# Kernel optimization log

Hardware: AMD Instinct MI355X
Metric: run time of the kernel (lower is better)

Reference implementation:

```python
import jax, jax.numpy as jnp
import numpy as np

EPS = 1e-5
NUM_HEAD = 8
HEAD_DIM = 64
SCALE = HEAD_DIM ** -0.5


def setup_inputs() -> dict:
    key = jax.random.key(0)
    ks = jax.random.split(key, 3)
    b, n, dim = 4, 2048, 512
    inner = NUM_HEAD * HEAD_DIM  # 512
    x = jax.random.normal(ks[0], (b, n, dim), dtype=jnp.float32)
    ln_w = jnp.ones((dim,), jnp.float32)
    ln_b = jnp.zeros((dim,), jnp.float32)
    qkv_w = jax.random.normal(ks[1], (3 * inner, dim), jnp.float32) * (dim ** -0.5)
    qkv_b = jnp.zeros((3 * inner,), jnp.float32)
    out_w = jax.random.normal(ks[2], (dim, inner), jnp.float32) * (inner ** -0.5)
    out_b = jnp.zeros((dim,), jnp.float32)
    return {"x": x, "ln_w": ln_w, "ln_b": ln_b, "qkv_w": qkv_w,
            "qkv_b": qkv_b, "out_w": out_w, "out_b": out_b}


def reference(x, ln_w, ln_b, qkv_w, qkv_b, out_w, out_b):
    b, n, dim = x.shape
    # Pre-norm LayerNorm
    mu = jnp.mean(x, axis=-1, keepdims=True)
    var = jnp.mean(jnp.square(x - mu), axis=-1, keepdims=True)
    xn = (x - mu) * jax.lax.rsqrt(var + EPS) * ln_w + ln_b
    # QKV projection (torch Linear: y = x @ W.T + b)
    qkv = xn @ qkv_w.T + qkv_b  # [b, n, 3*inner]
    q, k, v = jnp.split(qkv, 3, axis=-1)
    def heads(t):  # [b, n, inner] -> [b, h, n, d]
        return t.reshape(b, n, NUM_HEAD, HEAD_DIM).transpose(0, 2, 1, 3)
    q, k, v = heads(q), heads(k), heads(v)
    # Naive full attention (materializes [b, h, n, n])
    dots = jnp.einsum('bhqd,bhkd->bhqk', q, k) * SCALE
    attn = jax.nn.softmax(dots, axis=-1)
    o = jnp.einsum('bhqk,bhkd->bhqd', attn, v)
    o = o.transpose(0, 2, 1, 3).reshape(b, n, NUM_HEAD * HEAD_DIM)
    return o @ out_w.T + out_b
```

## Files before the change

### kernel.cpp

```cpp
#include <hip/hip_runtime.h>

typedef __attribute__((ext_vector_type(8))) short bf16x8;
typedef __attribute__((ext_vector_type(4))) float floatx4;
typedef __attribute__((ext_vector_type(16))) float floatx16;
typedef __attribute__((ext_vector_type(4))) unsigned int uintx4;

#define B_    4
#define N_    2048
#define DIM_  512
#define NH_   8
#define HD_   64
#define SCALE_ 0.125f
#define SL2E_ (0.125f * 1.44269504f)

__device__ __forceinline__ unsigned short f32_to_bf16(float f) {
    return (unsigned short)((__float_as_uint(f) + 0x8000u) >> 16);
}

__device__ __forceinline__ float bf16_to_f32(unsigned short u) {
    return __uint_as_float(((unsigned int)u) << 16);
}

__device__ __forceinline__ floatx4 mfma16(bf16x8 a, bf16x8 b, floatx4 c) {
    return __builtin_amdgcn_mfma_f32_16x16x32_bf16(a, b, c, 0, 0, 0);
}

__device__ __forceinline__ floatx16 mfma32(bf16x8 a, bf16x8 b, floatx16 c) {
    return __builtin_amdgcn_mfma_f32_32x32x16_bf16(a, b, c, 0, 0, 0);
}

__device__ __forceinline__ floatx4 fzero4() {
    floatx4 z = {0.f, 0.f, 0.f, 0.f};
    return z;
}

__device__ __forceinline__ floatx16 fzero16() {
    floatx16 z;
#pragma unroll
    for (int i = 0; i < 16; i++) z[i] = 0.f;
    return z;
}

__device__ __forceinline__ unsigned int cvt_pk_bf16(float lo, float hi) {
    unsigned int r;
    asm("v_cvt_pk_bf16_f32 %0, %1, %2" : "=v"(r) : "v"(lo), "v"(hi));
    return r;
}

__device__ __forceinline__ void async16(const unsigned short* g, unsigned short* l) {
    __builtin_amdgcn_global_load_lds((const __attribute__((address_space(1))) void*)g,
                                     (__attribute__((address_space(3))) void*)l,
                                     16, 0, 0);
}

__global__ __launch_bounds__(256) void ln_cvt_kernel(const float* __restrict__ x,
                                                     const float* __restrict__ w,
                                                     const float* __restrict__ b,
                                                     unsigned short* __restrict__ xn,
                                                     const float* __restrict__ srcA,
                                                     const float* __restrict__ srcB,
                                                     unsigned short* __restrict__ dstA,
                                                     unsigned short* __restrict__ dstB) {
    const int NWQ = 3 * DIM_ * DIM_;
    if (blockIdx.x < 2048) {
        int wv = threadIdx.x >> 6;
        int lane = threadIdx.x & 63;
        int row = blockIdx.x * 4 + wv;
        const float4* xr = (const float4*)(x + (size_t)row * DIM_);
        float4 v0 = xr[lane * 2];
        float4 v1 = xr[lane * 2 + 1];
        float s  = (v0.x + v0.y + v0.z + v0.w) + (v1.x + v1.y + v1.z + v1.w);
        float sq = v0.x*v0.x + v0.y*v0.y + v0.z*v0.z + v0.w*v0.w +
                   v1.x*v1.x + v1.y*v1.y + v1.z*v1.z + v1.w*v1.w;
#pragma unroll
        for (int off = 1; off < 64; off <<= 1) {
            s  += __shfl_xor(s, off, 64);
            sq += __shfl_xor(sq, off, 64);
        }
        float mu   = s * (1.f / DIM_);
        float var  = sq * (1.f / DIM_) - mu * mu;
        float rstd = rsqrtf(var + 1e-5f);
        float4 w0 = ((const float4*)w)[lane * 2];
        float4 w1 = ((const float4*)w)[lane * 2 + 1];
        float4 b0 = ((const float4*)b)[lane * 2];
        float4 b1 = ((const float4*)b)[lane * 2 + 1];
        float y[8];
        y[0] = (v0.x - mu) * rstd * w0.x + b0.x;
        y[1] = (v0.y - mu) * rstd * w0.y + b0.y;
        y[2] = (v0.z - mu) * rstd * w0.z + b0.z;
        y[3] = (v0.w - mu) * rstd * w0.w + b0.w;
        y[4] = (v1.x - mu) * rstd * w1.x + b1.x;
        y[5] = (v1.y - mu) * rstd * w1.y + b1.y;
        y[6] = (v1.z - mu) * rstd * w1.z + b1.z;
        y[7] = (v1.w - mu) * rstd * w1.w + b1.w;
        uint4 pk;
        pk.x = (unsigned int)f32_to_bf16(y[0]) | ((unsigned int)f32_to_bf16(y[1]) << 16);
        pk.y = (unsigned int)f32_to_bf16(y[2]) | ((unsigned int)f32_to_bf16(y[3]) << 16);
        pk.z = (unsigned int)f32_to_bf16(y[4]) | ((unsigned int)f32_to_bf16(y[5]) << 16);
        pk.w = (unsigned int)f32_to_bf16(y[6]) | ((unsigned int)f32_to_bf16(y[7]) << 16);
        ((uint4*)(xn + (size_t)row * DIM_))[lane] = pk;
    } else {
        int e0 = ((blockIdx.x - 2048) * 256 + threadIdx.x) * 8;
        const float* src;
        unsigned short* dst;
        if (e0 < NWQ) { src = srcA + e0; dst = dstA + e0; }
        else          { src = srcB + (e0 - NWQ); dst = dstB + (e0 - NWQ); }
        float4 u0 = ((const float4*)src)[0];
        float4 u1 = ((const float4*)src)[1];
        uint4 pk;
        pk.x = (unsigned int)f32_to_bf16(u0.x) | ((unsigned int)f32_to_bf16(u0.y) << 16);
        pk.y = (unsigned int)f32_to_bf16(u0.z) | ((unsigned int)f32_to_bf16(u0.w) << 16);
        pk.z = (unsigned int)f32_to_bf16(u1.x) | ((unsigned int)f32_to_bf16(u1.y) << 16);
        pk.w = (unsigned int)f32_to_bf16(u1.z) | ((unsigned int)f32_to_bf16(u1.w) << 16);
        *(uint4*)dst = pk;
    }
}

#define GEMM_CORE512(A_, B_ptr, am0, bn0)                                           \
    __shared__ unsigned short Alds[2][128][32];                                     \
    __shared__ unsigned short Blds[2][128][32];                                     \
    int tid = threadIdx.x, lane = tid & 63, wid = tid >> 6;                         \
    int l15 = lane & 15, quad = lane >> 4;                                          \
    int wmloc = (wid >> 1) * 32, wnloc = (wid & 1) * 64;                            \
    int sr = lane >> 2;                                                             \
    int sc = (lane & 3) * 8;                                                        \
    int srow0 = 16 * wid;                                                           \
    floatx4 acc[2][4];                                                              \
    _Pragma("unroll")                                                               \
    for (int i = 0; i < 2; i++)                                                     \
        _Pragma("unroll")                                                           \
        for (int j = 0; j < 4; j++) acc[i][j] = fzero4();                           \
    int buf = 0;                                                                    \
    async16(A_ + (size_t)(am0 + srow0 + sr) * DIM_ + sc, &Alds[0][srow0][0]);       \
    async16(B_ptr + (size_t)(bn0 + srow0 + sr) * DIM_ + sc, &Blds[0][srow0][0]);    \
    __syncthreads();                                                                \
    for (int t = 0; t < 16; t++) {                                                  \
        if (t < 15) {                                                               \
            int k0 = (t + 1) * 32;                                                  \
            async16(A_ + (size_t)(am0 + srow0 + sr) * DIM_ + k0 + sc,               \
                    &Alds[buf ^ 1][srow0][0]);                                      \
            async16(B_ptr + (size_t)(bn0 + srow0 + sr) * DIM_ + k0 + sc,            \
                    &Blds[buf ^ 1][srow0][0]);                                      \
        }                                                                           \
        bf16x8 av[2], bv[4];                                                        \
        _Pragma("unroll")                                                           \
        for (int i = 0; i < 2; i++)                                                 \
            av[i] = *(const bf16x8*)(&Alds[buf][wmloc + 16 * i + l15][quad * 8]);   \
        _Pragma("unroll")                                                           \
        for (int j = 0; j < 4; j++)                                                 \
            bv[j] = *(const bf16x8*)(&Blds[buf][wnloc + 16 * j + l15][quad * 8]);   \
        _Pragma("unroll")                                                           \
        for (int i = 0; i < 2; i++)                                                 \
            _Pragma("unroll")                                                       \
            for (int j = 0; j < 4; j++)                                             \
                acc[i][j] = mfma16(av[i], bv[j], acc[i][j]);                        \
        __syncthreads();                                                            \
        buf ^= 1;                                                                   \
    }

__global__ __launch_bounds__(512, 6) void qkv_gemm(const unsigned short* __restrict__ A,
                                                   const unsigned short* __restrict__ Bw,
                                                   const float* __restrict__ bias,
                                                   unsigned short* __restrict__ Qh,
                                                   unsigned short* __restrict__ Kh,
                                                   unsigned short* __restrict__ Vt) {
    int am0 = blockIdx.x * 128, bn0 = blockIdx.y * 128;
    GEMM_CORE512(A, Bw, am0, bn0)

    if (bn0 >= 1024) {
        unsigned short* sc_ = &Alds[0][0][0] + wid * (16 * 40);
        int m0 = am0 + wmloc;
        int bidx = m0 >> 11;
        int t0 = m0 & 2047;
#pragma unroll
        for (int j = 0; j < 4; j++) {
            float bias_n = bias[bn0 + wnloc + 16 * j + l15];
#pragma unroll
            for (int i = 0; i < 2; i++)
#pragma unroll
                for (int r = 0; r < 4; r++)
                    sc_[l15 * 40 + 16 * i + quad * 4 + r] =
                        f32_to_bf16(acc[i][j][r] + bias_n);
            int nr = lane >> 2;
            int rem = (bn0 - 1024) + wnloc + 16 * j + nr;
            int head = rem >> 6, d = rem & 63;
            bf16x8 vv = *(const bf16x8*)(sc_ + nr * 40 + (lane & 3) * 8);
            *(bf16x8*)(Vt + ((size_t)(bidx * NH_ + head) * HD_ + d) * N_ +
                       t0 + (lane & 3) * 8) = vv;
        }
    } else {
#pragma unroll
        for (int i = 0; i < 2; i++) {
#pragma unroll
            for (int j = 0; j < 4; j++) {
                int n = bn0 + wnloc + 16 * j + l15;
                float bias_n = bias[n];
                int which = n >> 9;
                int rem = n & 511;
                int head = rem >> 6;
                int d = rem & 63;
#pragma unroll
                for (int r = 0; r < 4; r++) {
                    int m = am0 + wmloc + 16 * i + quad * 4 + r;
                    int b = m >> 11;
                    int t = m & 2047;
                    float val = acc[i][j][r] + bias_n;
                    if (which == 0) {
                        Qh[((size_t)(b * NH_ + head) * N_ + t) * HD_ + d] =
                            f32_to_bf16(val * SL2E_);
                    } else {
                        Kh[((size_t)(b * NH_ + head) * N_ + t) * HD_ + d] =
                            f32_to_bf16(val);
                    }
                }
            }
        }
    }
}

__global__ __launch_bounds__(256, 4) void out_gemm_fused(const unsigned short* __restrict__ Opart,
                                                         const float* __restrict__ lpart,
                                                         const unsigned short* __restrict__ Bw,
                                                         const float* __restrict__ bias,
                                                         float* __restrict__ out) {
    __shared__ unsigned short Alds[2][64][36];
    __shared__ unsigned short Blds[2][128][32];
    int tid = threadIdx.x, lane = tid & 63, wid = tid >> 6;
    int l15 = lane & 15, quad = lane >> 4;
    int wmloc = (wid >> 1) * 32, wnloc = (wid & 1) * 64;
    int am0 = blockIdx.x * 64, bn0 = blockIdx.y * 128;

    int arow = tid >> 2;
    int ac8 = (tid & 3) * 8;
    int token = am0 + arow;
    int bb = token >> 11;
    const size_t LSTR = (size_t)B_ * NH_ * N_;
    const size_t OSTR = (size_t)B_ * N_ * DIM_;
    const unsigned short* arow0 = Opart + (size_t)token * DIM_;
    const unsigned short* arow1 = arow0 + OSTR;

    int sr = lane >> 2;
    int sc = (lane & 3) * 8;

    floatx4 acc[2][4];
#pragma unroll
    for (int i = 0; i < 2; i++)
#pragma unroll
        for (int j = 0; j < 4; j++) acc[i][j] = fzero4();

#define STAGE_A(BUF, T)                                                         \
    {                                                                           \
        int k0 = (T) * 32;                                                      \
        int head = k0 >> 6;                                                     \
        size_t li = (size_t)(bb * NH_ + head) * N_ + (token & 2047);            \
        float l1 = lpart[li];                                                   \
        float l2 = lpart[LSTR + li];                                            \
        float inv = 1.f / (l1 + l2);                                            \
        float w1 = l1 * inv, w2 = l2 * inv;                                     \
        bf16x8 o0 = *(const bf16x8*)(arow0 + k0 + ac8);                         \
        bf16x8 o1 = *(const bf16x8*)(arow1 + k0 + ac8);                         \
        bf16x8 pk;                                                              \
        _Pragma("unroll")                                                       \
        for (int e = 0; e < 8; e++)                                             \
            pk[e] = (short)f32_to_bf16(                                         \
                w1 * bf16_to_f32((unsigned short)o0[e]) +                       \
                w2 * bf16_to_f32((unsigned short)o1[e]));                       \
        *(bf16x8*)(&Alds[BUF][arow][ac8]) = pk;                                 \
    }

#define STAGE_B(BUF, T)                                                         \
    {                                                                           \
        int k0 = (T) * 32;                                                      \
        _Pragma("unroll")                                                       \
        for (int i = 0; i < 2; i++) {                                           \
            int r0 = 32 * wid + 16 * i;                                         \
            async16(Bw + (size_t)(bn0 + r0 + sr) * DIM_ + k0 + sc,              \
                    &Blds[BUF][r0][0]);                                         \
        }                                                                       \
    }

    STAGE_B(0, 0)
    STAGE_A(0, 0)
    __syncthreads();
    int buf = 0;
    for (int t = 0; t < 16; t++) {
        if (t < 15) {
            STAGE_B(buf ^ 1, t + 1)
            STAGE_A(buf ^ 1, t + 1)
        }
        bf16x8 av[2], bv[4];
#pragma unroll
        for (int i = 0; i < 2; i++)
            av[i] = *(const bf16x8*)(&Alds[buf][wmloc + 16 * i + l15][quad * 8]);
#pragma unroll
        for (int j = 0; j < 4; j++)
            bv[j] = *(const bf16x8*)(&Blds[buf][wnloc + 16 * j + l15][quad * 8]);
#pragma unroll
        for (int i = 0; i < 2; i++)
#pragma unroll
            for (int j = 0; j < 4; j++)
                acc[i][j] = mfma16(av[i], bv[j], acc[i][j]);
        __syncthreads();
        buf ^= 1;
    }
#undef STAGE_A
#undef STAGE_B

#pragma unroll
    for (int i = 0; i < 2; i++) {
#pragma unroll
        for (int j = 0; j < 4; j++) {
            int n = bn0 + wnloc + 16 * j + l15;
            float bias_n = bias[n];
#pragma unroll
            for (int r = 0; r < 4; r++) {
                int m = am0 + wmloc + 16 * i + quad * 4 + r;
                out[(size_t)m * DIM_ + n] = acc[i][j][r] + bias_n;
            }
        }
    }
}

__global__ __launch_bounds__(512, 4) void attn_kernel(const unsigned short* __restrict__ Qh,
                                                      const unsigned short* __restrict__ Kh,
                                                      const unsigned short* __restrict__ Vtg,
                                                      unsigned short* __restrict__ Opart,
                                                      float* __restrict__ lpart) {
    int bh = blockIdx.y;
    int b = bh >> 3, head = bh & 7;
    int qt = blockIdx.x;
    int split = blockIdx.z;
    int kv0 = split << 10;
    int tid = threadIdx.x, lane = tid & 63, w = tid >> 6;
    int l31 = lane & 31, hi = lane >> 5;
    int xr = l31 & 7;

    const unsigned short* Qp = Qh + (size_t)bh * N_ * HD_;
    const unsigned short* Kg = Kh + (size_t)bh * N_ * HD_;
    const unsigned short* Vg = Vtg + (size_t)bh * HD_ * N_;

    int q0 = qt * 256 + w * 32;

    bf16x8 aQ[4];
    {
        const unsigned short* qrow = Qp + (size_t)(q0 + l31) * HD_ + hi * 8;
#pragma unroll
        for (int t = 0; t < 4; t++)
            aQ[t] = *(const bf16x8*)(qrow + 16 * t);
    }

    __shared__ unsigned short KV[2][2][64][64];
    __shared__ float l_sm[8][32];

    int srow = lane >> 3;
    int scol = ((lane & 7) ^ srow) * 8;

    const char* ptc[4];
#pragma unroll
    for (int t = 0; t < 4; t++)
        ptc[t] = (const char*)&KV[0][0][l31][(((2 * t + hi) ^ xr) * 8)];

    const unsigned short* kSrc = Kg + (size_t)(kv0 + 8 * w + srow) * HD_ + scol;
    const unsigned short* vSrc = Vg + (size_t)(8 * w + srow) * N_ + kv0 + scol;

#define STAGE_KV(BUF, IT)                                                       \
    {                                                                           \
        async16(kSrc + (size_t)(IT) * 64 * HD_, &KV[BUF][0][8 * w][0]);         \
        async16(vSrc + (size_t)(IT) * 64, &KV[BUF][1][8 * w][0]);               \
    }

    floatx16 of[2];
    of[0] = fzero16();
    of[1] = fzero16();
    float lsA = 0.f, lsB = 0.f;

#define COMPUTE(BUF)                                                            \
    {                                                                           \
        bf16x8 pa[4];                                                           \
        _Pragma("unroll")                                                       \
        for (int tau = 0; tau < 2; tau++) {                                     \
            bf16x8 kf[4];                                                       \
            _Pragma("unroll")                                                   \
            for (int t = 0; t < 4; t++)                                         \
                kf[t] = *(const bf16x8*)(ptc[t] + (BUF) * 16384 + tau * 4096);  \
            floatx16 acc = fzero16();                                           \
            __builtin_amdgcn_s_setprio(1);                                      \
            _Pragma("unroll")                                                   \
            for (int t = 0; t < 4; t++)                                         \
                acc = mfma32(kf[t], aQ[t], acc);                                \
            __builtin_amdgcn_s_setprio(0);                                      \
            float p[16];                                                        \
            _Pragma("unroll")                                                   \
            for (int r = 0; r < 16; r += 2) {                                   \
                p[r]     = __builtin_amdgcn_exp2f(acc[r]);                      \
                p[r + 1] = __builtin_amdgcn_exp2f(acc[r + 1]);                  \
                lsA += p[r];                                                    \
                lsB += p[r + 1];                                                \
            }                                                                   \
            unsigned int a0 = cvt_pk_bf16(p[0], p[1]);                          \
            unsigned int b0 = cvt_pk_bf16(p[4], p[5]);                          \
            unsigned int a1 = cvt_pk_bf16(p[2], p[3]);                          \
            unsigned int b1 = cvt_pk_bf16(p[6], p[7]);                          \
            unsigned int a2 = cvt_pk_bf16(p[8], p[9]);                          \
            unsigned int b2 = cvt_pk_bf16(p[12], p[13]);                        \
            unsigned int a3 = cvt_pk_bf16(p[10], p[11]);                        \
            unsigned int b3 = cvt_pk_bf16(p[14], p[15]);                        \
            asm("v_permlane32_swap_b32 %0, %1" : "+v"(a0), "+v"(b0));           \
            asm("v_permlane32_swap_b32 %0, %1" : "+v"(a1), "+v"(b1));           \
            asm("v_permlane32_swap_b32 %0, %1" : "+v"(a2), "+v"(b2));           \
            asm("v_permlane32_swap_b32 %0, %1" : "+v"(a3), "+v"(b3));           \
            uintx4 f0 = {a0, a1, b0, b1};                                       \
            uintx4 f1 = {a2, a3, b2, b3};                                       \
            pa[2 * tau]     = __builtin_bit_cast(bf16x8, f0);                   \
            pa[2 * tau + 1] = __builtin_bit_cast(bf16x8, f1);                   \
        }                                                                       \
        __builtin_amdgcn_s_setprio(1);                                          \
        _Pragma("unroll")                                                       \
        for (int s = 0; s < 4; s++) {                                           \
            _Pragma("unroll")                                                   \
            for (int dt = 0; dt < 2; dt++) {                                    \
                bf16x8 vf = *(const bf16x8*)(ptc[s] + (BUF) * 16384 + 8192 +    \
                                             dt * 4096);                        \
                of[dt] = mfma32(pa[s], vf, of[dt]);                             \
            }                                                                   \
        }                                                                       \
        __builtin_amdgcn_s_setprio(0);                                          \
    }

    STAGE_KV(0, 0)
    __syncthreads();

    for (int it2 = 0; it2 < 8; it2++) {
        int it = it2 * 2;
        STAGE_KV(1, it + 1)
        COMPUTE(0)
        __syncthreads();
        if (it2 < 7) STAGE_KV(0, it + 2)
        COMPUTE(1)
        __syncthreads();
    }
#undef STAGE_KV
#undef COMPUTE

    float lsum = lsA + lsB;
    lsum += __shfl_xor(lsum, 32, 64);
    if (hi == 0) {
        l_sm[w][l31] = __builtin_amdgcn_rcpf(lsum);
        lpart[(size_t)split * B_ * NH_ * N_ + (size_t)bh * N_ + q0 + l31] = lsum;
    }
    asm volatile("s_waitcnt lgkmcnt(0)" ::: "memory");

    unsigned short* Od = Opart + (size_t)split * B_ * N_ * DIM_;
#pragma unroll
    for (int r = 0; r < 16; r++) {
        int qr = (r & 3) + 8 * (r >> 2) + 4 * hi;
        float inv = l_sm[w][qr];
        int token = q0 + qr;
        size_t base = ((size_t)b * N_ + token) * DIM_ + (size_t)head * HD_;
#pragma unroll
        for (int dt = 0; dt < 2; dt++)
            Od[base + 32 * dt + l31] = f32_to_bf16(of[dt][r] * inv);
    }
}

extern "C" void kernel_launch(void* const* d_in, const int* in_sizes, int n_in,
                              void* d_out, int out_size, void* d_ws, size_t ws_size,
                              hipStream_t stream) {
    const float* x     = (const float*)d_in[0];
    const float* ln_w  = (const float*)d_in[1];
    const float* ln_b  = (const float*)d_in[2];
    const float* qkv_w = (const float*)d_in[3];
    const float* qkv_b = (const float*)d_in[4];
    const float* out_w = (const float*)d_in[5];
    const float* out_b = (const float*)d_in[6];
    float* out = (float*)d_out;

    char* ws = (char*)d_ws;
    const size_t TOK = (size_t)B_ * N_;
    unsigned short* xn    = (unsigned short*)ws;  ws += TOK * DIM_ * 2;
    unsigned short* wq_bf = (unsigned short*)ws;  ws += (size_t)3 * DIM_ * DIM_ * 2;
    unsigned short* wo_bf = (unsigned short*)ws;  ws += (size_t)DIM_ * DIM_ * 2;
    unsigned short* Qh    = (unsigned short*)ws;  ws += TOK * DIM_ * 2;
    unsigned short* Kh    = (unsigned short*)ws;  ws += TOK * DIM_ * 2;
    unsigned short* Vt    = (unsigned short*)ws;  ws += TOK * DIM_ * 2;
    unsigned short* Opart = (unsigned short*)ws;  ws += (size_t)2 * TOK * DIM_ * 2;
    float*          lpart = (float*)ws;           ws += (size_t)2 * B_ * NH_ * N_ * 4;

    ln_cvt_kernel<<<2048 + 512, 256, 0, stream>>>(x, ln_w, ln_b, xn,
                                                  qkv_w, out_w, wq_bf, wo_bf);
    qkv_gemm<<<dim3(TOK / 128, (3 * DIM_) / 128), 512, 0, stream>>>(xn, wq_bf, qkv_b, Qh, Kh, Vt);
    attn_kernel<<<dim3(N_ / 256, B_ * NH_, 2), 512, 0, stream>>>(Qh, Kh, Vt, Opart, lpart);
    out_gemm_fused<<<dim3(TOK / 64, DIM_ / 128), 256, 0, stream>>>(Opart, lpart, wo_bf, out_b, out);
}
```

Before: 153.5 us.

## Deepen K/V async staging to four LDS buffers with vmcnt-based waits

The attention inner loop moves from double buffering to a four-buffer ring, with three tiles in flight ahead of compute. Full __syncthreads is replaced by explicit s_waitcnt vmcnt counts plus raw s_barrier, so later loads can remain outstanding while the current tile is consumed. This aims to hide global-load latency better, but doubles LDS use per block, which may lower occupancy, and relies on correct manual vmcnt accounting.

```diff
diff --git a/kernel.cpp b/kernel.cpp
--- a/kernel.cpp
+++ b/kernel.cpp
@@ -349,7 +349,7 @@
             aQ[t] = *(const bf16x8*)(qrow + 16 * t);
     }
 
-    __shared__ unsigned short KV[2][2][64][64];
+    __shared__ unsigned short KV[4][2][64][64];
     __shared__ float l_sm[8][32];
 
     int srow = lane >> 3;
@@ -368,6 +368,9 @@
         async16(kSrc + (size_t)(IT) * 64 * HD_, &KV[BUF][0][8 * w][0]);         \
         async16(vSrc + (size_t)(IT) * 64, &KV[BUF][1][8 * w][0]);               \
     }
+
+#define VMW(N)  asm volatile("s_waitcnt vmcnt(" #N ")" ::: "memory")
+#define RBAR()  asm volatile("s_barrier" ::: "memory")
 
     floatx16 of[2];
     of[0] = fzero16();
@@ -427,20 +430,34 @@
         __builtin_amdgcn_s_setprio(0);                                          \
     }
 
+#define ITER(BUF, VN, SBUF, STILE, DOSTAGE)                                     \
+    VMW(VN);                                                                    \
+    RBAR();                                                                     \
+    __builtin_amdgcn_sched_barrier(0);                                          \
+    COMPUTE(BUF)                                                                \
+    RBAR();                                                                     \
+    if (DOSTAGE) STAGE_KV(SBUF, STILE)
+
     STAGE_KV(0, 0)
-    __syncthreads();
-
-    for (int it2 = 0; it2 < 8; it2++) {
-        int it = it2 * 2;
-        STAGE_KV(1, it + 1)
-        COMPUTE(0)
-        __syncthreads();
-        if (it2 < 7) STAGE_KV(0, it + 2)
-        COMPUTE(1)
-        __syncthreads();
-    }
+    STAGE_KV(1, 1)
+    STAGE_KV(2, 2)
+
+    for (int g = 0; g < 3; g++) {
+        int base = g * 4;
+        ITER(0, 4, 3, base + 3, 1);
+        ITER(1, 4, 0, base + 4, 1);
+        ITER(2, 4, 1, base + 5, 1);
+        ITER(3, 4, 2, base + 6, 1);
+    }
+    ITER(0, 4, 3, 15, 1);
+    ITER(1, 4, 0, 0, 0);
+    ITER(2, 2, 0, 0, 0);
+    ITER(3, 0, 0, 0, 0);
+#undef ITER
 #undef STAGE_KV
 #undef COMPUTE
+#undef VMW
+#undef RBAR
 
     float lsum = lsA + lsB;
     lsum += __shfl_xor(lsum, 32, 64);
```

Measured after the change: 154.7 us. No clear change (+0.8%).

## Process two query chunks per wave in attention and vectorize Q/K epilogue stores

Applied to the files above, without the earlier changes.

Each attention wave now handles 64 query rows instead of 32, so every K/V tile read from LDS is reused for two query chunks. This halves the grid and the K/V staging traffic per query. The cost is higher register pressure, with launch bounds lowered to 2 blocks per CU. Separately, the QKV GEMM epilogue for Q/K now stages results in LDS and writes 16-byte vectors per row instead of scattered 2-byte stores.

```diff
diff --git a/kernel.cpp b/kernel.cpp
--- a/kernel.cpp
+++ b/kernel.cpp
@@ -189,30 +189,31 @@
                        t0 + (lane & 3) * 8) = vv;
         }
     } else {
+        unsigned short* sc2 = &Alds[0][0][0] + wid * 1024;
+        int n0 = bn0 + wnloc;
+        int which = n0 >> 9;
+        int head = (n0 & 511) >> 6;
+        unsigned short* dstBase = (which == 0) ? Qh : Kh;
+        float mul = (which == 0) ? SL2E_ : 1.f;
 #pragma unroll
         for (int i = 0; i < 2; i++) {
 #pragma unroll
             for (int j = 0; j < 4; j++) {
-                int n = bn0 + wnloc + 16 * j + l15;
-                float bias_n = bias[n];
-                int which = n >> 9;
-                int rem = n & 511;
-                int head = rem >> 6;
-                int d = rem & 63;
-#pragma unroll
-                for (int r = 0; r < 4; r++) {
-                    int m = am0 + wmloc + 16 * i + quad * 4 + r;
-                    int b = m >> 11;
-                    int t = m & 2047;
-                    float val = acc[i][j][r] + bias_n;
-                    if (which == 0) {
-                        Qh[((size_t)(b * NH_ + head) * N_ + t) * HD_ + d] =
-                            f32_to_bf16(val * SL2E_);
-                    } else {
-                        Kh[((size_t)(b * NH_ + head) * N_ + t) * HD_ + d] =
-                            f32_to_bf16(val);
-                    }
-                }
+                float bias_n = bias[n0 + 16 * j + l15];
+#pragma unroll
+                for (int r = 0; r < 4; r++)
+                    sc2[(quad * 4 + r) * 64 + 16 * j + l15] =
+                        f32_to_bf16((acc[i][j][r] + bias_n) * mul);
+            }
+            asm volatile("s_waitcnt lgkmcnt(0)" ::: "memory");
+#pragma unroll
+            for (int h = 0; h < 2; h++) {
+                int tl = 8 * h + (lane >> 3);
+                int m = am0 + wmloc + 16 * i + tl;
+                int bb2 = m >> 11, tt = m & 2047;
+                bf16x8 row = *(const bf16x8*)(sc2 + tl * 64 + (lane & 7) * 8);
+                *(bf16x8*)(dstBase + ((size_t)(bb2 * NH_ + head) * N_ + tt) * HD_ +
+                           (lane & 7) * 8) = row;
             }
         }
     }
@@ -321,7 +322,7 @@
     }
 }
 
-__global__ __launch_bounds__(512, 4) void attn_kernel(const unsigned short* __restrict__ Qh,
+__global__ __launch_bounds__(512, 2) void attn_kernel(const unsigned short* __restrict__ Qh,
                                                       const unsigned short* __restrict__ Kh,
                                                       const unsigned short* __restrict__ Vtg,
                                                       unsigned short* __restrict__ Opart,
@@ -339,18 +340,19 @@
     const unsigned short* Kg = Kh + (size_t)bh * N_ * HD_;
     const unsigned short* Vg = Vtg + (size_t)bh * HD_ * N_;
 
-    int q0 = qt * 256 + w * 32;
-
-    bf16x8 aQ[4];
-    {
-        const unsigned short* qrow = Qp + (size_t)(q0 + l31) * HD_ + hi * 8;
+    int q0 = qt * 512 + w * 64;
+
+    bf16x8 aQ[2][4];
+#pragma unroll
+    for (int qc = 0; qc < 2; qc++) {
+        const unsigned short* qrow = Qp + (size_t)(q0 + 32 * qc + l31) * HD_ + hi * 8;
 #pragma unroll
         for (int t = 0; t < 4; t++)
-            aQ[t] = *(const bf16x8*)(qrow + 16 * t);
+            aQ[qc][t] = *(const bf16x8*)(qrow + 16 * t);
     }
 
     __shared__ unsigned short KV[2][2][64][64];
-    __shared__ float l_sm[8][32];
+    __shared__ float l_sm[8][64];
 
     int srow = lane >> 3;
     int scol = ((lane & 7) ^ srow) * 8;
@@ -369,50 +371,56 @@
         async16(vSrc + (size_t)(IT) * 64, &KV[BUF][1][8 * w][0]);               \
     }
 
-    floatx16 of[2];
-    of[0] = fzero16();
-    of[1] = fzero16();
-    float lsA = 0.f, lsB = 0.f;
+    floatx16 of[2][2];
+#pragma unroll
+    for (int qc = 0; qc < 2; qc++)
+#pragma unroll
+        for (int dt = 0; dt < 2; dt++) of[qc][dt] = fzero16();
+    float ls[2][2] = {{0.f, 0.f}, {0.f, 0.f}};
+    const floatx16 z16 = fzero16();
 
 #define COMPUTE(BUF)                                                            \
     {                                                                           \
-        bf16x8 pa[4];                                                           \
+        bf16x8 pa[2][4];                                                        \
         _Pragma("unroll")                                                       \
         for (int tau = 0; tau < 2; tau++) {                                     \
             bf16x8 kf[4];                                                       \
             _Pragma("unroll")                                                   \
             for (int t = 0; t < 4; t++)                                         \
                 kf[t] = *(const bf16x8*)(ptc[t] + (BUF) * 16384 + tau * 4096);  \
-            floatx16 acc = fzero16();                                           \
-            __builtin_amdgcn_s_setprio(1);                                      \
             _Pragma("unroll")                                                   \
-            for (int t = 0; t < 4; t++)                                         \
-                acc = mfma32(kf[t], aQ[t], acc);                                \
-            __builtin_amdgcn_s_setprio(0);                                      \
-            float p[16];                                                        \
-            _Pragma("unroll")                                                   \
-            for (int r = 0; r < 16; r += 2) {                                   \
-                p[r]     = __builtin_amdgcn_exp2f(acc[r]);                      \
-                p[r + 1] = __builtin_amdgcn_exp2f(acc[r + 1]);                  \
-                lsA += p[r];                                                    \
-                lsB += p[r + 1];                                                \
+            for (int qc = 0; qc < 2; qc++) {                                    \
+                __builtin_amdgcn_s_setprio(1);                                  \
+                floatx16 acc = mfma32(kf[0], aQ[qc][0], z16);                   \
+                acc = mfma32(kf[1], aQ[qc][1], acc);                            \
+                acc = mfma32(kf[2], aQ[qc][2], acc);                            \
+                acc = mfma32(kf[3], aQ[qc][3], acc);                            \
+                __builtin_amdgcn_s_setprio(0);                                  \
+                float p[16];                                                    \
+                _Pragma("unroll")                                               \
+                for (int r = 0; r < 16; r += 2) {                               \
+                    p[r]     = __builtin_amdgcn_exp2f(acc[r]);                  \
+                    p[r + 1] = __builtin_amdgcn_exp2f(acc[r + 1]);              \
+                    ls[qc][0] += p[r];                                          \
+                    ls[qc][1] += p[r + 1];                                      \
+                }                                                               \
+                unsigned int a0 = cvt_pk_bf16(p[0], p[1]);                      \
+                unsigned int b0 = cvt_pk_bf16(p[4], p[5]);                      \
+                unsigned int a1 = cvt_pk_bf16(p[2], p[3]);                      \
+                unsigned int b1 = cvt_pk_bf16(p[6], p[7]);                      \
+                unsigned int a2 = cvt_pk_bf16(p[8], p[9]);                      \
+                unsigned int b2 = cvt_pk_bf16(p[12], p[13]);                    \
+                unsigned int a3 = cvt_pk_bf16(p[10], p[11]);                    \
+                unsigned int b3 = cvt_pk_bf16(p[14], p[15]);                    \
+                asm("v_permlane32_swap_b32 %0, %1" : "+v"(a0), "+v"(b0));       \
+                asm("v_permlane32_swap_b32 %0, %1" : "+v"(a1), "+v"(b1));       \
+                asm("v_permlane32_swap_b32 %0, %1" : "+v"(a2), "+v"(b2));       \
+                asm("v_permlane32_swap_b32 %0, %1" : "+v"(a3), "+v"(b3));       \
+                uintx4 f0 = {a0, a1, b0, b1};                                   \
+                uintx4 f1 = {a2, a3, b2, b3};                                   \
+                pa[qc][2 * tau]     = __builtin_bit_cast(bf16x8, f0);           \
+                pa[qc][2 * tau + 1] = __builtin_bit_cast(bf16x8, f1);           \
             }                                                                   \
-            unsigned int a0 = cvt_pk_bf16(p[0], p[1]);                          \
-            unsigned int b0 = cvt_pk_bf16(p[4], p[5]);                          \
-            unsigned int a1 = cvt_pk_bf16(p[2], p[3]);                          \
-            unsigned int b1 = cvt_pk_bf16(p[6], p[7]);                          \
-            unsigned int a2 = cvt_pk_bf16(p[8], p[9]);                          \
-            unsigned int b2 = cvt_pk_bf16(p[12], p[13]);                        \
-            unsigned int a3 = cvt_pk_bf16(p[10], p[11]);                        \
-            unsigned int b3 = cvt_pk_bf16(p[14], p[15]);                        \
-            asm("v_permlane32_swap_b32 %0, %1" : "+v"(a0), "+v"(b0));           \
-            asm("v_permlane32_swap_b32 %0, %1" : "+v"(a1), "+v"(b1));           \
-            asm("v_permlane32_swap_b32 %0, %1" : "+v"(a2), "+v"(b2));           \
-            asm("v_permlane32_swap_b32 %0, %1" : "+v"(a3), "+v"(b3));           \
-            uintx4 f0 = {a0, a1, b0, b1};                                       \
-            uintx4 f1 = {a2, a3, b2, b3};                                       \
-            pa[2 * tau]     = __builtin_bit_cast(bf16x8, f0);                   \
-            pa[2 * tau + 1] = __builtin_bit_cast(bf16x8, f1);                   \
         }                                                                       \
         __builtin_amdgcn_s_setprio(1);                                          \
         _Pragma("unroll")                                                       \
@@ -421,7 +429,8 @@
             for (int dt = 0; dt < 2; dt++) {                                    \
                 bf16x8 vf = *(const bf16x8*)(ptc[s] + (BUF) * 16384 + 8192 +    \
                                              dt * 4096);                        \
-                of[dt] = mfma32(pa[s], vf, of[dt]);                             \
+                of[0][dt] = mfma32(pa[0][s], vf, of[0][dt]);                    \
+                of[1][dt] = mfma32(pa[1][s], vf, of[1][dt]);                    \
             }                                                                   \
         }                                                                       \
         __builtin_amdgcn_s_setprio(0);                                          \
@@ -442,11 +451,15 @@
 #undef STAGE_KV
 #undef COMPUTE
 
-    float lsum = lsA + lsB;
-    lsum += __shfl_xor(lsum, 32, 64);
-    if (hi == 0) {
-        l_sm[w][l31] = __builtin_amdgcn_rcpf(lsum);
-        lpart[(size_t)split * B_ * NH_ * N_ + (size_t)bh * N_ + q0 + l31] = lsum;
+#pragma unroll
+    for (int qc = 0; qc < 2; qc++) {
+        float lsum = ls[qc][0] + ls[qc][1];
+        lsum += __shfl_xor(lsum, 32, 64);
+        if (hi == 0) {
+            l_sm[w][32 * qc + l31] = __builtin_amdgcn_rcpf(lsum);
+            lpart[(size_t)split * B_ * NH_ * N_ + (size_t)bh * N_ +
+                  q0 + 32 * qc + l31] = lsum;
+        }
     }
     asm volatile("s_waitcnt lgkmcnt(0)" ::: "memory");
 
@@ -454,12 +467,15 @@
 #pragma unroll
     for (int r = 0; r < 16; r++) {
         int qr = (r & 3) + 8 * (r >> 2) + 4 * hi;
-        float inv = l_sm[w][qr];
-        int token = q0 + qr;
-        size_t base = ((size_t)b * N_ + token) * DIM_ + (size_t)head * HD_;
-#pragma unroll
-        for (int dt = 0; dt < 2; dt++)
-            Od[base + 32 * dt + l31] = f32_to_bf16(of[dt][r] * inv);
+#pragma unroll
+        for (int qc = 0; qc < 2; qc++) {
+            float inv = l_sm[w][32 * qc + qr];
+            int token = q0 + 32 * qc + qr;
+            size_t base = ((size_t)b * N_ + token) * DIM_ + (size_t)head * HD_;
+#pragma unroll
+            for (int dt = 0; dt < 2; dt++)
+                Od[base + 32 * dt + l31] = f32_to_bf16(of[qc][dt][r] * inv);
+        }
     }
 }
 
@@ -489,6 +505,6 @@
     ln_cvt_kernel<<<2048 + 512, 256, 0, stream>>>(x, ln_w, ln_b, xn,
                                                   qkv_w, out_w, wq_bf, wo_bf);
     qkv_gemm<<<dim3(TOK / 128, (3 * DIM_) / 128), 512, 0, stream>>>(xn, wq_bf, qkv_b, Qh, Kh, Vt);
-    attn_kernel<<<dim3(N_ / 256, B_ * NH_, 2), 512, 0, stream>>>(Qh, Kh, Vt, Opart, lpart);
+    attn_kernel<<<dim3(N_ / 512, B_ * NH_, 2), 512, 0, stream>>>(Qh, Kh, Vt, Opart, lpart);
     out_gemm_fused<<<dim3(TOK / 64, DIM_ / 128), 256, 0, stream>>>(Opart, lpart, wo_bf, out_b, out);
 }
```

Result: no change. 152.2 us (-0.8%).
